# Performance work log

Hardware: AMD Instinct MI355X
Metric: run time of the kernel (lower is better)

## Reference

```python
import jax, jax.numpy as jnp
import numpy as np

B, D, C = 8192, 2048, 1000

def setup_inputs() -> dict:
    key = jax.random.key(0)
    k1, k2, k3 = jax.random.split(key, 3)
    x = jax.random.normal(k1, (B, D), dtype=jnp.float32)
    W = jax.random.normal(k2, (D, C), dtype=jnp.float32) * (1.0 / np.sqrt(D))
    b = jax.random.normal(k3, (C,), dtype=jnp.float32) * 0.01
    return {"x": x, "W": W, "b": b}

def reference(x, W, b):
    # inner classifier: logits out[b, c]
    out = jnp.dot(x, W) + b  # [B, C]
    # leave-one-out logsumexp per class, fused:
    # lse_k = logsumexp(out[:, != k]) = lse_all + log1p(-exp(out_k - lse_all))
    lse = jax.nn.logsumexp(out, axis=1, keepdims=True)  # [B, 1]
    loo = lse + jnp.log1p(-jnp.exp(out - lse))           # [B, C]
    # c_out = -loo; return c_out + out
    return out - loo
```

## Files before the change

kernel.cpp:

```cpp
#include <hip/hip_runtime.h>
#include <hip/hip_bf16.h>
#include <math.h>

#define BDIM 8192
#define DDIM 2048
#define CDIM 1000
#define BK   64

#define WS_P0_OFFSET  4194304ULL
#define WS_P1_OFFSET  20578304ULL

typedef __attribute__((ext_vector_type(8))) short short8;
typedef __attribute__((ext_vector_type(4))) float floatx4;

__device__ __forceinline__ unsigned short f2bf(float f) {
    union { float f; unsigned u; } a; a.f = f;
    unsigned u = a.u;
    u = (u + 0x7fff + ((u >> 16) & 1)) >> 16;
    return (unsigned short)u;
}

__device__ __forceinline__ float bf2f(unsigned short h) {
    union { unsigned u; float f; } a; a.u = ((unsigned)h) << 16;
    return a.f;
}

__device__ __forceinline__ void async_copy16(const void* gp, void* lp) {
    __builtin_amdgcn_global_load_lds(
        (const __attribute__((address_space(1))) void*)gp,
        (__attribute__((address_space(3))) void*)lp,
        16, 0, 0);
}

__global__ __launch_bounds__(256) void cvt_w_kernel(
    const float* __restrict__ W, unsigned short* __restrict__ Bt)
{
    __shared__ float tile[32][33];
    const int b2 = blockIdx.x;
    const int t  = threadIdx.x;
    const int k0 = (b2 & 63) * 32;
    const int n0 = (b2 >> 6) * 32;
    const int tx = t & 31, ty = t >> 5;
    #pragma unroll
    for (int i = 0; i < 4; i++) {
        int k = k0 + ty + i * 8;
        int n = n0 + tx;
        tile[ty + i * 8][tx] = (n < CDIM) ? W[(size_t)k * CDIM + n] : 0.0f;
    }
    __syncthreads();
    #pragma unroll
    for (int i = 0; i < 4; i++) {
        int n = n0 + ty + i * 8;
        int k = k0 + tx;
        Bt[(size_t)n * DDIM + k] = f2bf(tile[tx][ty + i * 8]);
    }
}


#define HBUF (256 * BK)

#define STAGE_B2(BASE, EXT, KO)                                               \
    do {                                                                      \
        _Pragma("unroll")                                                     \
        for (int h = 0; h < 2; h++) {                                         \
            const int row_ = rB0 + (EXT) + h * 128;                           \
            async_copy16(gB + (size_t)row_ * DDIM + (KO),                     \
                         (BASE) + row_ * BK + c8);                            \
        }                                                                     \
    } while (0)

#define ISSUE_A(SL, EXT, KO)                                                  \
    do {                                                                      \
        const float* p0_ = gAf + (size_t)(q0 + (EXT)) * DDIM + (KO);          \
        const float* p1_ = p0_ + (size_t)128 * DDIM;                          \
        axr[(SL) + 0] = *(const float4*)(p0_);                                \
        axr[(SL) + 1] = *(const float4*)(p0_ + 4);                            \
        axr[(SL) + 2] = *(const float4*)(p1_);                                \
        axr[(SL) + 3] = *(const float4*)(p1_ + 4);                            \
    } while (0)

#define WRITE_A(BASE, SL, EXT)                                                \
    do {                                                                      \
        _Pragma("unroll")                                                     \
        for (int r_ = 0; r_ < 2; r_++) {                                      \
            const int row_ = q0 + (EXT) + r_ * 128;                           \
            float4 lo_ = axr[(SL) + r_ * 2];                                  \
            float4 hi_ = axr[(SL) + r_ * 2 + 1];                              \
            short8 pk_;                                                       \
            pk_[0] = (short)f2bf(lo_.x); pk_[1] = (short)f2bf(lo_.y);         \
            pk_[2] = (short)f2bf(lo_.z); pk_[3] = (short)f2bf(lo_.w);         \
            pk_[4] = (short)f2bf(hi_.x); pk_[5] = (short)f2bf(hi_.y);         \
            pk_[6] = (short)f2bf(hi_.z); pk_[7] = (short)f2bf(hi_.w);         \
            *(short8*)((BASE) + row_ * BK + csw) = pk_;                       \
        }                                                                     \
    } while (0)

#define LOADA_(BASE, MQ)                                                      \
    do {                                                                      \
        _Pragma("unroll")                                                     \
        for (int mf = 0; mf < 4; mf++) {                                      \
            const int r_ = (arA + (MQ) * 64 + mf * 16) * BK;                  \
            af[mf][0] = *(const short8*)((BASE) + r_ + xorb0);                \
            af[mf][1] = *(const short8*)((BASE) + r_ + xorb1);                \
        }                                                                     \
    } while (0)

#define LOADB_(BASE, NQ, BF)                                                  \
    do {                                                                      \
        _Pragma("unroll")                                                     \
        for (int nf = 0; nf < 2; nf++) {                                      \
            const int r_ = (arB + (NQ) * 32 + nf * 16) * BK;                  \
            BF[nf][0] = *(const short8*)((BASE) + r_ + xorb0);                \
            BF[nf][1] = *(const short8*)((BASE) + r_ + xorb1);                \
        }                                                                     \
    } while (0)

#define MMAC(MQ, NQ, BF)                                                      \
    do {                                                                      \
        __builtin_amdgcn_s_setprio(1);                                        \
        _Pragma("unroll")                                                     \
        for (int mf = 0; mf < 4; mf++) {                                      \
            _Pragma("unroll")                                                 \
            for (int nf = 0; nf < 2; nf++) {                                  \
                floatx4 c_ = acc[(MQ) * 4 + mf][(NQ) * 2 + nf];               \
                c_ = __builtin_amdgcn_mfma_f32_16x16x32_bf16(                 \
                    af[mf][0], BF[nf][0], c_, 0, 0, 0);                       \
                c_ = __builtin_amdgcn_mfma_f32_16x16x32_bf16(                 \
                    af[mf][1], BF[nf][1], c_, 0, 0, 0);                       \
                acc[(MQ) * 4 + mf][(NQ) * 2 + nf] = c_;                       \
            }                                                                 \
        }                                                                     \
        __builtin_amdgcn_s_setprio(0);                                        \
    } while (0)

#define RAW_BARRIER() asm volatile("s_barrier" ::: "memory")
#define WAIT_VM(N)    asm volatile("s_waitcnt vmcnt(" #N ")" ::: "memory")
#define WAIT_LGKM0()  asm volatile("s_waitcnt lgkmcnt(0)" ::: "memory")

__global__ __launch_bounds__(512) void gemm8_kernel(
    const float* __restrict__ X,
    const unsigned short* __restrict__ Bt,
    unsigned short* __restrict__ P0, unsigned short* __restrict__ P1)
{
    __shared__ unsigned short As[2 * HBUF];
    __shared__ unsigned short Bs[2 * HBUF];

    const int t    = threadIdx.x;
    const int wave = t >> 6;
    const int lane = t & 63;
    const int wm   = wave >> 2;
    const int wn   = wave & 3;
    const int quad = lane >> 4;
    const int l16  = lane & 15;

    const int L    = blockIdx.x;
    const int g    = (L & 7) * 32 + (L >> 3);
    const int z    = g & 1;
    const int tid2 = g >> 1;
    const int mBase = (tid2 >> 2) * 256;
    const int nBase = (tid2 & 3) * 256;
    const int kBase = z * (DDIM / 2);
    const int NTt   = (DDIM / 2) / BK;

    const int c8  = (t & 7) << 3;
    const int q0  = t >> 3;
    const int csw = (((t & 7) ^ (q0 & 7)) << 3);
    const int rB0 = q0 + (q0 & 32);
    const float* gAf = X + (size_t)mBase * DDIM + kBase + ((t & 7) << 3);
    const unsigned short* gB = Bt + (size_t)nBase * DDIM + kBase + csw;

    const int xorb0 = ((0 * 4 + quad) ^ (l16 & 7)) << 3;
    const int xorb1 = ((1 * 4 + quad) ^ (l16 & 7)) << 3;
    const int arA = wm * 128 + l16;
    const int arB = wn * 64 + l16;

    floatx4 acc[8][4] = {};
    short8 af[4][2], bf0[2][2], bf1[2][2];
    float4 axr[8];

    ISSUE_A(0, 0, 0);
    ISSUE_A(4, 64, 0);
    WAIT_VM(0);
    WRITE_A(As, 0, 0);
    WRITE_A(As, 4, 64);
    STAGE_B2(Bs, 0, 0);
    STAGE_B2(Bs, 32, 0);
    ISSUE_A(0, 0, BK);
    ISSUE_A(4, 64, BK);
    WAIT_VM(0);
    WRITE_A(As + HBUF, 0, 0);
    WRITE_A(As + HBUF, 4, 64);
    STAGE_B2(Bs + HBUF, 0, BK);
    STAGE_B2(Bs + HBUF, 32, BK);
    WAIT_LGKM0();
    RAW_BARRIER();
    LOADA_(As, 0);
    LOADB_(Bs, 0, bf0);
    WAIT_LGKM0();
    RAW_BARRIER();

    for (int j = 0; j < NTt; j++) {
        const int bo = (j & 1) * HBUF;
        unsigned short* const cA = (unsigned short*)As + bo;
        unsigned short* const cB = (unsigned short*)Bs + bo;
        const unsigned short* const nA = (const unsigned short*)As + (bo ^ HBUF);
        const unsigned short* const nB = (const unsigned short*)Bs + (bo ^ HBUF);
        const int  ko2 = (j + 2) * BK;
        const bool s2  = (j + 2 < NTt);

        if (s2) ISSUE_A(0, 0, ko2);
        MMAC(0, 0, bf0);
        LOADB_(cB, 1, bf1);
        RAW_BARRIER();

        if (s2) STAGE_B2(cB, 0, ko2);
        if (s2) ISSUE_A(4, 64, ko2);
        MMAC(0, 1, bf1);
        LOADA_(cA, 1);
        RAW_BARRIER();

        if (s2) {
            STAGE_B2(cB, 32, ko2);
            WAIT_VM(8);
            WRITE_A(cA, 0, 0);
        }
        MMAC(1, 0, bf0);
        RAW_BARRIER();

        if (s2) {
            WAIT_VM(4);
            WRITE_A(cA, 4, 64);
        } else {
            WAIT_VM(0);
        }
        MMAC(1, 1, bf1);
        if (j + 1 < NTt) { LOADA_(nA, 0); LOADB_(nB, 0, bf0); }
        WAIT_LGKM0();
        RAW_BARRIER();
    }

    unsigned short* P = z ? P1 : P0;
    #pragma unroll
    for (int mfg = 0; mfg < 8; mfg++) {
        const int row0 = mBase + wm * 128 + mfg * 16 + quad * 4;
        #pragma unroll
        for (int nfg = 0; nfg < 4; nfg++) {
            const int col = nBase + wn * 64 + nfg * 16 + l16;
            if (col < CDIM) {
                #pragma unroll
                for (int rg = 0; rg < 4; rg++)
                    P[(size_t)(row0 + rg) * CDIM + col] = f2bf(acc[mfg][nfg][rg]);
            }
        }
    }
}

__global__ __launch_bounds__(256) void lse_kernel(
    float* __restrict__ out,
    const unsigned short* P0, const unsigned short* P1,
    const float* __restrict__ bias, int split)
{
    const int row = blockIdx.x;
    const int t   = threadIdx.x;
    __shared__ float red[8];

    const bool valid = t < (CDIM / 4);
    const int c0 = t * 4;

    float4 v = make_float4(-INFINITY, -INFINITY, -INFINITY, -INFINITY);
    float4 e = make_float4(0.f, 0.f, 0.f, 0.f);
    if (valid) {
        if (split) {
            ushort4 p0 = *(const ushort4*)(P0 + (size_t)row * CDIM + c0);
            ushort4 p1 = *(const ushort4*)(P1 + (size_t)row * CDIM + c0);
            v.x = bf2f(p0.x) + bf2f(p1.x);
            v.y = bf2f(p0.y) + bf2f(p1.y);
            v.z = bf2f(p0.z) + bf2f(p1.z);
            v.w = bf2f(p0.w) + bf2f(p1.w);
        } else {
            v = *(const float4*)(out + (size_t)row * CDIM + c0);
        }
        float4 bb = *(const float4*)(bias + c0);
        v.x += bb.x; v.y += bb.y; v.z += bb.z; v.w += bb.w;
    }

    float m = fmaxf(fmaxf(v.x, v.y), fmaxf(v.z, v.w));
    #pragma unroll
    for (int off = 32; off > 0; off >>= 1)
        m = fmaxf(m, __shfl_down(m, off, 64));
    const int wave = t >> 6;
    if ((t & 63) == 0) red[wave] = m;
    __syncthreads();
    if (t == 0) red[4] = fmaxf(fmaxf(red[0], red[1]), fmaxf(red[2], red[3]));
    __syncthreads();
    const float M = red[4];

    float s = 0.f;
    if (valid) {
        e.x = expf(v.x - M); e.y = expf(v.y - M);
        e.z = expf(v.z - M); e.w = expf(v.w - M);
        s = e.x + e.y + e.z + e.w;
    }
    #pragma unroll
    for (int off = 32; off > 0; off >>= 1)
        s += __shfl_down(s, off, 64);
    if ((t & 63) == 0) red[wave] = s;
    __syncthreads();
    if (t == 0) red[4] = red[0] + red[1] + red[2] + red[3];
    __syncthreads();
    const float S    = red[4];
    const float lse  = M + logf(S);
    const float invS = 1.0f / S;

    if (valid) {
        float4 o;
        o.x = (v.x - lse) - log1pf(-e.x * invS);
        o.y = (v.y - lse) - log1pf(-e.y * invS);
        o.z = (v.z - lse) - log1pf(-e.z * invS);
        o.w = (v.w - lse) - log1pf(-e.w * invS);
        *(float4*)(out + (size_t)row * CDIM + c0) = o;
    }
}

extern "C" void kernel_launch(void* const* d_in, const int* in_sizes, int n_in,
                              void* d_out, int out_size, void* d_ws, size_t ws_size,
                              hipStream_t stream) {
    const float* x = (const float*)d_in[0];
    const float* W = (const float*)d_in[1];
    const float* b = (const float*)d_in[2];
    float* out = (float*)d_out;

    unsigned short* Bt = (unsigned short*)d_ws;
    unsigned short* P0 = (unsigned short*)((char*)d_ws + WS_P0_OFFSET);
    unsigned short* P1 = (unsigned short*)((char*)d_ws + WS_P1_OFFSET);

    cvt_w_kernel<<<2048, 256, 0, stream>>>(W, Bt);

    gemm8_kernel<<<256, 512, 0, stream>>>(x, Bt, P0, P1);

    lse_kernel<<<BDIM, 256, 0, stream>>>(out, P0, P1, b, 1);
}
```

Before: 185.8 us.

## Deepen A-tile prefetch to three stages with per-piece fp32 loads

Splits the fp32 A-tile global loads into four pieces, each issued three k-tiles ahead and converted to bf16 into LDS one piece per MMA phase, so global load latency overlaps more MFMA work. Loads are clamped at the last tile instead of being predicated, which adds a few redundant loads at the tail. It also adds a launch-bounds occupancy hint of 2 blocks per CU and removes the unused non-split path from the LSE kernel. The occupancy hint may cap registers and cause spills given the large accumulator array.

```diff
diff --git a/kernel.cpp b/kernel.cpp
--- a/kernel.cpp
+++ b/kernel.cpp
@@ -69,30 +69,25 @@
         }                                                                     \
     } while (0)
 
-#define ISSUE_A(SL, EXT, KO)                                                  \
-    do {                                                                      \
-        const float* p0_ = gAf + (size_t)(q0 + (EXT)) * DDIM + (KO);          \
-        const float* p1_ = p0_ + (size_t)128 * DDIM;                          \
-        axr[(SL) + 0] = *(const float4*)(p0_);                                \
-        axr[(SL) + 1] = *(const float4*)(p0_ + 4);                            \
-        axr[(SL) + 2] = *(const float4*)(p1_);                                \
-        axr[(SL) + 3] = *(const float4*)(p1_ + 4);                            \
-    } while (0)
-
-#define WRITE_A(BASE, SL, EXT)                                                \
-    do {                                                                      \
-        _Pragma("unroll")                                                     \
-        for (int r_ = 0; r_ < 2; r_++) {                                      \
-            const int row_ = q0 + (EXT) + r_ * 128;                           \
-            float4 lo_ = axr[(SL) + r_ * 2];                                  \
-            float4 hi_ = axr[(SL) + r_ * 2 + 1];                              \
-            short8 pk_;                                                       \
-            pk_[0] = (short)f2bf(lo_.x); pk_[1] = (short)f2bf(lo_.y);         \
-            pk_[2] = (short)f2bf(lo_.z); pk_[3] = (short)f2bf(lo_.w);         \
-            pk_[4] = (short)f2bf(hi_.x); pk_[5] = (short)f2bf(hi_.y);         \
-            pk_[6] = (short)f2bf(hi_.z); pk_[7] = (short)f2bf(hi_.w);         \
-            *(short8*)((BASE) + row_ * BK + csw) = pk_;                       \
-        }                                                                     \
+#define ISSUE_P(P, KO)                                                        \
+    do {                                                                      \
+        const float* p_ = gAf +                                               \
+            (size_t)(q0 + ((P) >> 1) * 64 + ((P) & 1) * 128) * DDIM + (KO);   \
+        ax[P][0] = *(const float4*)(p_);                                      \
+        ax[P][1] = *(const float4*)(p_ + 4);                                  \
+    } while (0)
+
+#define WRITE_P(BASE, P)                                                      \
+    do {                                                                      \
+        const int row_ = q0 + ((P) >> 1) * 64 + ((P) & 1) * 128;              \
+        float4 lo_ = ax[P][0];                                                \
+        float4 hi_ = ax[P][1];                                                \
+        short8 pk_;                                                           \
+        pk_[0] = (short)f2bf(lo_.x); pk_[1] = (short)f2bf(lo_.y);             \
+        pk_[2] = (short)f2bf(lo_.z); pk_[3] = (short)f2bf(lo_.w);             \
+        pk_[4] = (short)f2bf(hi_.x); pk_[5] = (short)f2bf(hi_.y);             \
+        pk_[6] = (short)f2bf(hi_.z); pk_[7] = (short)f2bf(hi_.w);             \
+        *(short8*)((BASE) + row_ * BK + csw) = pk_;                           \
     } while (0)
 
 #define LOADA_(BASE, MQ)                                                      \
@@ -137,7 +132,7 @@
 #define WAIT_VM(N)    asm volatile("s_waitcnt vmcnt(" #N ")" ::: "memory")
 #define WAIT_LGKM0()  asm volatile("s_waitcnt lgkmcnt(0)" ::: "memory")
 
-__global__ __launch_bounds__(512) void gemm8_kernel(
+__global__ __launch_bounds__(512, 2) void gemm8_kernel(
     const float* __restrict__ X,
     const unsigned short* __restrict__ Bt,
     unsigned short* __restrict__ P0, unsigned short* __restrict__ P1)
@@ -176,22 +171,24 @@
 
     floatx4 acc[8][4] = {};
     short8 af[4][2], bf0[2][2], bf1[2][2];
-    float4 axr[8];
-
-    ISSUE_A(0, 0, 0);
-    ISSUE_A(4, 64, 0);
+    float4 ax[4][2];
+
+    ISSUE_P(0, 0); ISSUE_P(1, 0); ISSUE_P(2, 0); ISSUE_P(3, 0);
     WAIT_VM(0);
-    WRITE_A(As, 0, 0);
-    WRITE_A(As, 4, 64);
+    WRITE_P(As, 0); WRITE_P(As, 1); WRITE_P(As, 2); WRITE_P(As, 3);
+    ISSUE_P(0, BK); ISSUE_P(1, BK); ISSUE_P(2, BK); ISSUE_P(3, BK);
     STAGE_B2(Bs, 0, 0);
     STAGE_B2(Bs, 32, 0);
-    ISSUE_A(0, 0, BK);
-    ISSUE_A(4, 64, BK);
-    WAIT_VM(0);
-    WRITE_A(As + HBUF, 0, 0);
-    WRITE_A(As + HBUF, 4, 64);
+    WAIT_VM(4);
+    WRITE_P(As + HBUF, 0); WRITE_P(As + HBUF, 1);
+    WRITE_P(As + HBUF, 2); WRITE_P(As + HBUF, 3);
+    ISSUE_P(0, 2 * BK);
     STAGE_B2(Bs + HBUF, 0, BK);
+    ISSUE_P(1, 2 * BK);
     STAGE_B2(Bs + HBUF, 32, BK);
+    ISSUE_P(2, 2 * BK);
+    ISSUE_P(3, 2 * BK);
+    WAIT_VM(12);
     WAIT_LGKM0();
     RAW_BARRIER();
     LOADA_(As, 0);
@@ -205,39 +202,40 @@
         unsigned short* const cB = (unsigned short*)Bs + bo;
         const unsigned short* const nA = (const unsigned short*)As + (bo ^ HBUF);
         const unsigned short* const nB = (const unsigned short*)Bs + (bo ^ HBUF);
-        const int  ko2 = (j + 2) * BK;
-        const bool s2  = (j + 2 < NTt);
-
-        if (s2) ISSUE_A(0, 0, ko2);
+        const int koB = (j + 2 < NTt ? j + 2 : NTt - 1) * BK;
+        const int koA = (j + 3 < NTt ? j + 3 : NTt - 1) * BK;
+
         MMAC(0, 0, bf0);
         LOADB_(cB, 1, bf1);
+        WAIT_VM(10);
+        WRITE_P(cA, 0);
+        ISSUE_P(0, koA);
         RAW_BARRIER();
 
-        if (s2) STAGE_B2(cB, 0, ko2);
-        if (s2) ISSUE_A(4, 64, ko2);
+        STAGE_B2(cB, 0, koB);
         MMAC(0, 1, bf1);
         LOADA_(cA, 1);
+        WAIT_VM(10);
+        WRITE_P(cA, 1);
+        ISSUE_P(1, koA);
         RAW_BARRIER();
 
-        if (s2) {
-            STAGE_B2(cB, 32, ko2);
-            WAIT_VM(8);
-            WRITE_A(cA, 0, 0);
-        }
+        STAGE_B2(cB, 32, koB);
         MMAC(1, 0, bf0);
+        WAIT_VM(10);
+        WRITE_P(cA, 2);
+        ISSUE_P(2, koA);
         RAW_BARRIER();
 
-        if (s2) {
-            WAIT_VM(4);
-            WRITE_A(cA, 4, 64);
-        } else {
-            WAIT_VM(0);
-        }
         MMAC(1, 1, bf1);
+        WAIT_VM(10);
+        WRITE_P(cA, 3);
+        ISSUE_P(3, koA);
         if (j + 1 < NTt) { LOADA_(nA, 0); LOADB_(nB, 0, bf0); }
         WAIT_LGKM0();
         RAW_BARRIER();
     }
+    WAIT_VM(0);
 
     unsigned short* P = z ? P1 : P0;
     #pragma unroll
@@ -258,7 +256,7 @@
 __global__ __launch_bounds__(256) void lse_kernel(
     float* __restrict__ out,
     const unsigned short* P0, const unsigned short* P1,
-    const float* __restrict__ bias, int split)
+    const float* __restrict__ bias)
 {
     const int row = blockIdx.x;
     const int t   = threadIdx.x;
@@ -270,16 +268,12 @@
     float4 v = make_float4(-INFINITY, -INFINITY, -INFINITY, -INFINITY);
     float4 e = make_float4(0.f, 0.f, 0.f, 0.f);
     if (valid) {
-        if (split) {
-            ushort4 p0 = *(const ushort4*)(P0 + (size_t)row * CDIM + c0);
-            ushort4 p1 = *(const ushort4*)(P1 + (size_t)row * CDIM + c0);
-            v.x = bf2f(p0.x) + bf2f(p1.x);
-            v.y = bf2f(p0.y) + bf2f(p1.y);
-            v.z = bf2f(p0.z) + bf2f(p1.z);
-            v.w = bf2f(p0.w) + bf2f(p1.w);
-        } else {
-            v = *(const float4*)(out + (size_t)row * CDIM + c0);
-        }
+        ushort4 p0 = *(const ushort4*)(P0 + (size_t)row * CDIM + c0);
+        ushort4 p1 = *(const ushort4*)(P1 + (size_t)row * CDIM + c0);
+        v.x = bf2f(p0.x) + bf2f(p1.x);
+        v.y = bf2f(p0.y) + bf2f(p1.y);
+        v.z = bf2f(p0.z) + bf2f(p1.z);
+        v.w = bf2f(p0.w) + bf2f(p1.w);
         float4 bb = *(const float4*)(bias + c0);
         v.x += bb.x; v.y += bb.y; v.z += bb.z; v.w += bb.w;
     }
@@ -338,5 +332,5 @@
 
     gemm8_kernel<<<256, 512, 0, stream>>>(x, Bt, P0, P1);
 
-    lse_kernel<<<BDIM, 256, 0, stream>>>(out, P0, P1, b, 1);
-}
+    lse_kernel<<<BDIM, 256, 0, stream>>>(out, P0, P1, b);
+}
```

Result: slower. 202.1 us (+8.8%).
